# Kernel optimization log

Hardware: AMD Instinct MI355X
Metric: run time of the kernel (lower is better)

The kernel has to match this reference:

```python
import jax, jax.numpy as jnp
import numpy as np
from jax import lax

B, C, H, W = 4, 24, 128, 128
R = 7
NUM_CLASSES = 6
MAX_STEPS = 8


def _conv(x, w, b, pad):
    y = lax.conv_general_dilated(x, w, (1, 1), [(pad, pad), (pad, pad)],
                                 dimension_numbers=("NCHW", "OIHW", "NCHW"))
    return y + b[None, :, None, None]


def setup_inputs() -> dict:
    key = jax.random.key(0)
    ks = jax.random.split(key, 16)
    s = 0.05
    inp = {
        "depth_latent": jax.random.normal(ks[0], (B, C, H, W), jnp.float32),
        "texture_features": jax.random.normal(ks[1], (B, 3, H, W), jnp.float32),
        "class_labels": jax.random.randint(ks[2], (B,), 0, NUM_CLASSES),
        # texture_encoder
        "w_te1": jax.random.normal(ks[3], (64, 3, 3, 3), jnp.float32) * s,
        "b_te1": jnp.zeros((64,), jnp.float32),
        "w_te2": jax.random.normal(ks[4], (128, 64, 3, 3), jnp.float32) * s,
        "b_te2": jnp.zeros((128,), jnp.float32),
        # class embedding [num_classes, 128]
        "emb": jax.random.normal(ks[5], (NUM_CLASSES, 128), jnp.float32) * s,
        # fusion_layer: Conv2d(256,256,3) -> Conv2d(256, C*R*R, 1)
        "w_f1": jax.random.normal(ks[6], (256, 256, 3, 3), jnp.float32) * s,
        "b_f1": jnp.zeros((256,), jnp.float32),
        "w_f2": jax.random.normal(ks[7], (C * R * R, 256, 1, 1), jnp.float32) * s,
        "b_f2": jnp.zeros((C * R * R,), jnp.float32),
        # class_gate: Conv2d(128,64,3) -> Conv2d(64,num_classes,1)
        "w_g1": jax.random.normal(ks[8], (64, 128, 3, 3), jnp.float32) * s,
        "b_g1": jnp.zeros((64,), jnp.float32),
        "w_g2": jax.random.normal(ks[9], (NUM_CLASSES, 64, 1, 1), jnp.float32) * s,
        "b_g2": jnp.zeros((NUM_CLASSES,), jnp.float32),
        "class_intensity": jnp.ones((1, NUM_CLASSES, 1, 1), jnp.float32),
    }
    return inp


def _forward(depth_latent, texture_features, class_labels,
             w_te1, b_te1, w_te2, b_te2, emb,
             w_f1, b_f1, w_f2, b_f2,
             w_g1, b_g1, w_g2, b_g2, class_intensity):
    pad = R // 2
    # texture encoder
    tex = jax.nn.relu(_conv(texture_features, w_te1, b_te1, 1))
    tex = jax.nn.relu(_conv(tex, w_te2, b_te2, 1))  # [B,128,H,W]

    # 1-D integer class label path
    class_cond = jax.nn.one_hot(class_labels, NUM_CLASSES, dtype=jnp.float32)[:, :, None, None]  # [B,K,1,1]
    class_emb = emb[class_labels][:, :, None, None]  # [B,128,1,1]

    gate = jax.nn.sigmoid(_conv(jax.nn.relu(_conv(tex, w_g1, b_g1, 1)), w_g2, b_g2, 0))
    class_gate = gate * class_cond  # [B,K,H,W]

    fused = jnp.concatenate([tex, jnp.broadcast_to(class_emb, (tex.shape[0], 128, H, W))], axis=1)
    weights = _conv(jax.nn.relu(_conv(fused, w_f1, b_f1, 1)), w_f2, b_f2, 0)
    weights = weights.reshape(-1, C, R * R, H, W)

    intensity_map = (class_gate * class_intensity).sum(axis=1, keepdims=True)  # [B,1,H,W]
    weights = weights * intensity_map[:, :, None]  # [B,C,R*R,H,W]
    weights = jax.nn.softmax(weights, axis=2)

    def diffusion_step(lat):
        p = jnp.pad(lat, ((0, 0), (0, 0), (pad, pad), (pad, pad)), mode="edge")
        # unfold order: kernel row-major (i*R + j)
        windows = jnp.stack([p[:, :, i:i + H, j:j + W]
                             for i in range(R) for j in range(R)], axis=2)
        return (windows * weights).sum(axis=2)

    enhanced = lax.fori_loop(0, MAX_STEPS, lambda _, lat: diffusion_step(lat), depth_latent)

    condition_map = intensity_map * class_gate.sum(axis=1, keepdims=True)
    return enhanced, class_gate, condition_map


def reference(depth_latent, texture_features, class_labels,
              w_te1, b_te1, w_te2, b_te2, emb,
              w_f1, b_f1, w_f2, b_f2,
              w_g1, b_g1, w_g2, b_g2, class_intensity):
    return _forward(depth_latent, texture_features, class_labels,
                    w_te1, b_te1, w_te2, b_te2, emb,
                    w_f1, b_f1, w_f2, b_f2,
                    w_g1, b_g1, w_g2, b_g2, class_intensity)
```

## Files before the change

### kernel.cpp

```cpp
#include <hip/hip_runtime.h>
#include <hip/hip_bf16.h>
#include <stdint.h>

#define DINL __device__ __forceinline__

DINL float bf2f(__hip_bfloat16 v) { return __bfloat162float(v); }
DINL __hip_bfloat16 f2bf(float v) { return __float2bfloat16(v); }
DINL float bflo(unsigned int u) { return __uint_as_float(u << 16); }
DINL float bfhi(unsigned int u) { return __uint_as_float(u & 0xffff0000u); }

DINL float loadf(float v) { return v; }
DINL float loadf(__hip_bfloat16 v) { return __bfloat162float(v); }

typedef __attribute__((ext_vector_type(8))) short bf16x8;
typedef __attribute__((ext_vector_type(4))) float f32x4;

#define O_WTE1 0
#define O_WG2  1792
#define O_SS   2304
#define O_INT  11520
#define BO_W2B   308224u
#define BO_TE2B 1094656u
#define BO_WG1B 1242112u
#define BO_WF1B 1389568u
#define BO_TEX  4194304u
#define BO_F1   20971520u
#define BO_PING 54525952u
#define BO_PONG 60817408u
#define BO_W    67108864u
#define BO_T1   BO_W
#define BO_G1   (BO_W + 16777216u)

__global__ __launch_bounds__(256) void prep_kernel(
    const float* __restrict__ w_te1, const float* __restrict__ w_te2,
    const float* __restrict__ w_g1,  const float* __restrict__ w_f1,
    const float* __restrict__ w_f2,  const float* __restrict__ w_g2,
    const float* __restrict__ emb,   const int* __restrict__ labels,
    float* __restrict__ wsf)
{
  const int gid = blockIdx.x * 256 + threadIdx.x;
  const int stride = gridDim.x * 256;
  const int A0 = 1728, A1 = A0 + 393216, A2 = A1 + 73728, A3 = A2 + 73728,
            A4 = A3 + 294912, A5 = A4 + 384;
  __hip_bfloat16* w2b  = (__hip_bfloat16*)((char*)wsf + BO_W2B);
  __hip_bfloat16* te2b = (__hip_bfloat16*)((char*)wsf + BO_TE2B);
  __hip_bfloat16* g1b  = (__hip_bfloat16*)((char*)wsf + BO_WG1B);
  __hip_bfloat16* f1b  = (__hip_bfloat16*)((char*)wsf + BO_WF1B);
  for (int i = gid; i < A5; i += stride) {
    if (i < A0) {
      int s = i; int o = s / 27; int r = s - o * 27; int ic = r / 9; int t = r - ic * 9;
      wsf[O_WTE1 + (((o >> 5) * 3 + ic) * 9 + t) * 32 + (o & 31)] = w_te1[s];
    } else if (i < A1) {
      int s = i - A0;
      int j = s & 7; int lane = (s >> 3) & 63; int ks = (s >> 9) & 7;
      int mt = (s >> 12) & 3; int c = s >> 14;
      int tap = mt * 16 + (lane & 15);
      int k = ks * 32 + (lane >> 4) * 8 + j;
      float v = (tap < 49) ? w_f2[(c * 49 + tap) * 256 + k] : 0.f;
      w2b[s] = f2bf(v);
    } else if (i < A2) {
      int s = i - A1;
      int k = s & 31; int n = (s >> 5) & 63; int u = s >> 11;
      int t = u % 9; int v = u / 9; int kc = v & 1; int ocg = v >> 1;
      te2b[s] = f2bf(w_te2[((ocg * 64 + n) * 64 + kc * 32 + k) * 9 + t]);
    } else if (i < A3) {
      int s = i - A2;
      int k = s & 31; int n = (s >> 5) & 63; int u = s >> 11;
      int t = u % 9; int kc = u / 9;
      g1b[s] = f2bf(w_g1[(n * 128 + kc * 32 + k) * 9 + t]);
    } else if (i < A4) {
      int s = i - A3;
      int k = s & 31; int n = (s >> 5) & 63; int u = s >> 11;
      int t = u % 9; int v = u / 9; int kc = v & 3; int ocg = v >> 2;
      f1b[s] = f2bf(w_f1[((ocg * 64 + n) * 256 + kc * 32 + k) * 9 + t]);
    } else {
      int s = i - A4;
      wsf[O_WG2 + s] = w_g2[s];
    }
  }
  if (gid < 16384) {
    const int g = gid >> 4, slot = gid & 15;
    const int b = g >> 8, o = g & 255;
    const int lab = labels[b];
    float St[9];
#pragma unroll
    for (int t = 0; t < 9; ++t) St[t] = 0.f;
#pragma unroll 2
    for (int k = 0; k < 8; ++k) {
      const int i = slot * 8 + k;
      const float e = emb[lab * 128 + i];
      const float* wr = w_f1 + (size_t)(o * 256 + 128 + i) * 9;
#pragma unroll
      for (int t = 0; t < 9; ++t) St[t] += wr[t] * e;
    }
#pragma unroll
    for (int d = 1; d < 16; d <<= 1)
#pragma unroll
      for (int t = 0; t < 9; ++t) St[t] += __shfl_xor(St[t], d, 64);
    if (slot == 0) {
#pragma unroll
      for (int ch = 0; ch < 3; ++ch)
#pragma unroll
        for (int cw = 0; cw < 3; ++cw) {
          float sum = 0.f;
#pragma unroll
          for (int t = 0; t < 9; ++t) {
            int kh = t / 3, kw = t - kh * 3;
            bool ok = !(ch == 0 && kh == 0) && !(ch == 2 && kh == 2) &&
                      !(cw == 0 && kw == 0) && !(cw == 2 && kw == 2);
            if (ok) sum += St[t];
          }
          wsf[O_SS + g * 9 + ch * 3 + cw] = sum;
        }
    }
  }
}

template<typename TIn, int ICH, bool PIXMAJOR>
__global__ __launch_bounds__(256, 2) void conv3x3_kernel(
    const TIn* __restrict__ in, const float* __restrict__ wf,
    const float* __restrict__ bias,
    __hip_bfloat16* __restrict__ out, const int och_total)
{
  constexpr int CH = (ICH < 16) ? ICH : 16;
  constexpr int NCHUNK = ICH / CH;
  __shared__ TIn sIn[CH][18][20];
  const int tid = threadIdx.x;
  const int b = blockIdx.z;
  const int ob = blockIdx.y;
  const int och0 = ob * 32;
  const int tileY = blockIdx.x >> 3, tileX = blockIdx.x & 7;
  const int ty = tid >> 4, tx = tid & 15;
  const int h = tileY * 16 + ty, w = tileX * 16 + tx;
  const int h0 = tileY * 16 - 1, w0 = tileX * 16 - 1;

  float acc[32];
#pragma unroll
  for (int o = 0; o < 32; ++o) acc[o] = bias[och0 + o];

  for (int cc = 0; cc < NCHUNK; ++cc) {
    if (cc) __syncthreads();
    for (int e = tid; e < CH * 324; e += 256) {
      int ic = e / 324, r = e - ic * 324;
      int y = r / 18, x = r - y * 18;
      int gh = h0 + y, gw = w0 + x;
      TIn v = TIn(0.f);
      if ((unsigned)gh < 128u && (unsigned)gw < 128u)
        v = in[((b * ICH + cc * CH + ic) << 14) + (gh << 7) + gw];
      sIn[ic][y][x] = v;
    }
    __syncthreads();
#pragma unroll 1
    for (int ic = 0; ic < CH; ++ic) {
      const float* wrow = wf + (ob * ICH + cc * CH + ic) * 288;
#pragma unroll
      for (int t = 0; t < 9; ++t) {
        const int kh = t / 3, kw = t - kh * 3;
        const float v = loadf(sIn[ic][ty + kh][tx + kw]);
#pragma unroll
        for (int o = 0; o < 32; ++o)
          acc[o] = fmaf(wrow[t * 32 + o], v, acc[o]);
      }
    }
  }

  const int pix = (h << 7) + w;
  if constexpr (!PIXMAJOR) {
#pragma unroll
    for (int o = 0; o < 32; ++o)
      out[((b * och_total + och0 + o) << 14) + pix] = f2bf(fmaxf(acc[o], 0.f));
  } else {
    union { uint4 u4[4]; __hip_bfloat16 hh[32]; } pk;
#pragma unroll
    for (int o = 0; o < 32; ++o) pk.hh[o] = f2bf(fmaxf(acc[o], 0.f));
    uint4* dst = reinterpret_cast<uint4*>(out + ((size_t)(b << 14) + pix) * och_total + och0);
#pragma unroll
    for (int i = 0; i < 4; ++i) dst[i] = pk.u4[i];
  }
}

template<int ICH, bool ADD_SS>
__global__ __launch_bounds__(256, 2) void conv3x3_mfma_kernel(
    const __hip_bfloat16* __restrict__ in, const __hip_bfloat16* __restrict__ wb,
    const float* __restrict__ bias, const float* __restrict__ SS,
    __hip_bfloat16* __restrict__ out, const int och_total)
{
  constexpr int NKC = ICH / 32;
  __shared__ __hip_bfloat16 sH[324][40];
  __shared__ __hip_bfloat16 sW[9][64][40];
  const int tid = threadIdx.x, b = blockIdx.z, ocg = blockIdx.y;
  const int tileY = blockIdx.x >> 3, tileX = blockIdx.x & 7;
  const int h0 = tileY * 16 - 1, w0 = tileX * 16 - 1;
  const int wave = tid >> 6, lane = tid & 63, m16 = lane & 15, quad = lane >> 4;

  f32x4 acc[4][4];
#pragma unroll
  for (int i = 0; i < 4; ++i)
#pragma unroll
    for (int j = 0; j < 4; ++j) acc[i][j] = f32x4{0.f, 0.f, 0.f, 0.f};

  for (int kc = 0; kc < NKC; ++kc) {
    if (kc) __syncthreads();
    for (int e = tid; e < 1296; e += 256) {
      int pos = e >> 2, q = e & 3;
      int y = pos / 18, x = pos - y * 18;
      int gh = h0 + y, gw = w0 + x;
      uint4 v = uint4{0u, 0u, 0u, 0u};
      if ((unsigned)gh < 128u && (unsigned)gw < 128u)
        v = *(const uint4*)(in + ((size_t)((b << 14) + (gh << 7) + gw)) * ICH + kc * 32 + q * 8);
      *(uint4*)&sH[pos][q * 8] = v;
    }
    const uint4* wsrc = (const uint4*)(wb + ((size_t)(ocg * NKC + kc)) * 9 * 64 * 32);
    for (int e = tid; e < 2304; e += 256) {
      int q = e & 3, n = (e >> 2) & 63, t = e >> 8;
      *(uint4*)&sW[t][n][q * 8] = wsrc[e];
    }
    __syncthreads();
#pragma unroll
    for (int t = 0; t < 9; ++t) {
      const int dy = t / 3, dx = t - dy * 3;
      bf16x8 bfr[4];
#pragma unroll
      for (int nt = 0; nt < 4; ++nt)
        bfr[nt] = *(const bf16x8*)&sW[t][nt * 16 + m16][quad * 8];
#pragma unroll
      for (int mi = 0; mi < 4; ++mi) {
        const int py = wave * 4 + mi;
        const bf16x8 afr = *(const bf16x8*)&sH[(py + dy) * 18 + dx + m16][quad * 8];
#pragma unroll
        for (int nt = 0; nt < 4; ++nt)
          acc[mi][nt] = __builtin_amdgcn_mfma_f32_16x16x32_bf16(afr, bfr[nt], acc[mi][nt], 0, 0, 0);
      }
    }
  }

  float bv[4];
#pragma unroll
  for (int nt = 0; nt < 4; ++nt) bv[nt] = bias[ocg * 64 + nt * 16 + m16];
#pragma unroll
  for (int mi = 0; mi < 4; ++mi) {
    const int py = wave * 4 + mi;
    const int h = tileY * 16 + py;
    const int chc = (h == 0) ? 0 : ((h == 127) ? 2 : 1);
#pragma unroll
    for (int nt = 0; nt < 4; ++nt) {
      float sr0 = 0.f, sr1 = 0.f, sr2 = 0.f;
      if constexpr (ADD_SS) {
        const float* sp = SS + ((size_t)(b << 8) + (ocg * 64 + nt * 16 + m16)) * 9;
        sr0 = sp[chc * 3 + 0]; sr1 = sp[chc * 3 + 1]; sr2 = sp[chc * 3 + 2];
      }
      const int och = ocg * 64 + nt * 16 + m16;
#pragma unroll
      for (int r = 0; r < 4; ++r) {
        const int px = quad * 4 + r;
        const int w = tileX * 16 + px;
        float v = acc[mi][nt][r] + bv[nt];
        if constexpr (ADD_SS)
          v += (w == 0) ? sr0 : ((w == 127) ? sr2 : sr1);
        v = fmaxf(v, 0.f);
        out[((size_t)((b << 14) + (h << 7) + w)) * och_total + och] = f2bf(v);
      }
    }
  }
}

__global__ __launch_bounds__(256) void gate2_kernel(
    const __hip_bfloat16* __restrict__ g1, const float* __restrict__ wg2,
    const float* __restrict__ b_g2, const int* __restrict__ labels,
    const float* __restrict__ ci,
    float* __restrict__ out_cg, float* __restrict__ out_cond,
    float* __restrict__ inten)
{
  const int b = blockIdx.y;
  const int pix = blockIdx.x * 256 + threadIdx.x;
  float acc[6];
#pragma unroll
  for (int k = 0; k < 6; ++k) acc[k] = b_g2[k];
  const uint4* gp = (const uint4*)(g1 + ((size_t)((b << 14) + pix)) * 64);
#pragma unroll
  for (int i4 = 0; i4 < 8; ++i4) {
    const uint4 q = gp[i4];
    const float v0 = bflo(q.x), v1 = bfhi(q.x), v2 = bflo(q.y), v3 = bfhi(q.y);
    const float v4 = bflo(q.z), v5 = bfhi(q.z), v6 = bflo(q.w), v7 = bfhi(q.w);
#pragma unroll
    for (int k = 0; k < 6; ++k) {
      const float* wr = wg2 + k * 64 + i4 * 8;
      acc[k] = fmaf(wr[0], v0, acc[k]); acc[k] = fmaf(wr[1], v1, acc[k]);
      acc[k] = fmaf(wr[2], v2, acc[k]); acc[k] = fmaf(wr[3], v3, acc[k]);
      acc[k] = fmaf(wr[4], v4, acc[k]); acc[k] = fmaf(wr[5], v5, acc[k]);
      acc[k] = fmaf(wr[6], v6, acc[k]); acc[k] = fmaf(wr[7], v7, acc[k]);
    }
  }
  const int lab = labels[b];
  float gate[6], gl = 0.f;
#pragma unroll
  for (int k = 0; k < 6; ++k) {
    gate[k] = 1.f / (1.f + __expf(-acc[k]));
    gl = (k == lab) ? gate[k] : gl;
  }
  const float civ = ci[lab];
  const float it = gl * civ;
#pragma unroll
  for (int k = 0; k < 6; ++k)
    out_cg[((b * 6 + k) << 14) + pix] = (k == lab) ? gate[k] : 0.f;
  inten[(b << 14) + pix] = it;
  out_cond[(b << 14) + pix] = it * gl;
}

__global__ __launch_bounds__(256, 3) void gemm_softmax_kernel(
    const __hip_bfloat16* __restrict__ f1, const __hip_bfloat16* __restrict__ w2b,
    const float* __restrict__ b_f2, const float* __restrict__ inten,
    __hip_bfloat16* __restrict__ wout)
{
  __shared__ __hip_bfloat16 sW[2][8192];
  const int tid = threadIdx.x;
  const int pix0 = blockIdx.x * 128;
  const int c0 = blockIdx.y * 8;
  const int wave = tid >> 6, lane = tid & 63;
  const int n16 = lane & 15, quad = lane >> 4;
  const int p0 = pix0 + wave * 16 + n16;
  const int p1 = p0 + 64;

  bf16x8 bfr0[8], bfr1[8];
#pragma unroll
  for (int ks = 0; ks < 8; ++ks) {
    bfr0[ks] = *(const bf16x8*)(f1 + (size_t)p0 * 256 + ks * 32 + quad * 8);
    bfr1[ks] = *(const bf16x8*)(f1 + (size_t)p1 * 256 + ks * 32 + quad * 8);
  }

  const float s0v = inten[p0], s1v = inten[p1];
  const int ob0 = p0 >> 14, op0 = p0 & 16383;
  const int ob1 = p1 >> 14, op1 = p1 & 16383;

#define W2U(u) ((const uint4*)(w2b + ((((size_t)c0 + ((u) >> 1)) * 4 + (((u) & 1) << 1)) << 12)))

  {
    const uint4* s0 = W2U(0);
    uint4 t0[4];
#pragma unroll
    for (int j = 0; j < 4; ++j) t0[j] = s0[tid + j * 256];
    uint4* d0 = (uint4*)&sW[0][0];
#pragma unroll
    for (int j = 0; j < 4; ++j) d0[tid + j * 256] = t0[j];
  }
  __syncthreads();

#pragma unroll 1
  for (int cl = 0; cl < 8; ++cl) {
    const int c = c0 + cl;
    f32x4 ac0[4], ac1[4];
#pragma unroll
    for (int mt = 0; mt < 4; ++mt) { ac0[mt] = f32x4{0.f,0.f,0.f,0.f}; ac1[mt] = f32x4{0.f,0.f,0.f,0.f}; }

#pragma unroll
    for (int h = 0; h < 2; ++h) {
      const int u = cl * 2 + h;
      const uint4* sn = W2U(u < 15 ? u + 1 : 15);
      uint4 tn[4];
#pragma unroll
      for (int j = 0; j < 4; ++j) tn[j] = sn[tid + j * 256];

      const __hip_bfloat16* bufp = &sW[u & 1][0];
#pragma unroll
      for (int ks = 0; ks < 8; ++ks) {
        const bf16x8 a0 = *(const bf16x8*)(bufp + ((ks) * 64 + lane) * 8);
        const bf16x8 a1 = *(const bf16x8*)(bufp + ((8 + ks) * 64 + lane) * 8);
        ac0[h * 2 + 0] = __builtin_amdgcn_mfma_f32_16x16x32_bf16(a0, bfr0[ks], ac0[h * 2 + 0], 0, 0, 0);
        ac1[h * 2 + 0] = __builtin_amdgcn_mfma_f32_16x16x32_bf16(a0, bfr1[ks], ac1[h * 2 + 0], 0, 0, 0);
        ac0[h * 2 + 1] = __builtin_amdgcn_mfma_f32_16x16x32_bf16(a1, bfr0[ks], ac0[h * 2 + 1], 0, 0, 0);
        ac1[h * 2 + 1] = __builtin_amdgcn_mfma_f32_16x16x32_bf16(a1, bfr1[ks], ac1[h * 2 + 1], 0, 0, 0);
      }

      uint4* dn = (uint4*)&sW[(u + 1) & 1][0];
#pragma unroll
      for (int j = 0; j < 4; ++j) dn[tid + j * 256] = tn[j];
      __syncthreads();
    }

#pragma unroll
    for (int g = 0; g < 2; ++g) {
      f32x4* ac = g ? ac1 : ac0;
      const float s = g ? s1v : s0v;
      float mx = -3.4e38f;
#pragma unroll
      for (int mt = 0; mt < 4; ++mt)
#pragma unroll
        for (int r = 0; r < 4; ++r) {
          const int tap = mt * 16 + quad * 4 + r;
          const bool ok = tap < 49;
          const float lv = ok ? (ac[mt][r] + b_f2[c * 49 + (ok ? tap : 0)]) * s : -3.4e38f;
          ac[mt][r] = lv;
          mx = fmaxf(mx, lv);
        }
      mx = fmaxf(mx, __shfl_xor(mx, 16, 64));
      mx = fmaxf(mx, __shfl_xor(mx, 32, 64));
      float sum = 0.f;
#pragma unroll
      for (int mt = 0; mt < 4; ++mt)
#pragma unroll
        for (int r = 0; r < 4; ++r) {
          const float e = __expf(ac[mt][r] - mx);
          ac[mt][r] = e;
          sum += e;
        }
      sum += __shfl_xor(sum, 16, 64);
      sum += __shfl_xor(sum, 32, 64);
      const float rs = 1.f / sum;

      __hip_bfloat16* wo = wout + (((size_t)((g ? ob1 : ob0) * 24 + c) * 49) << 14) + (g ? op1 : op0);
#pragma unroll
      for (int mt = 0; mt < 4; ++mt)
#pragma unroll
        for (int r = 0; r < 4; ++r) {
          const int tap = mt * 16 + quad * 4 + r;
          if (tap < 49) wo[(size_t)tap << 14] = f2bf(ac[mt][r] * rs);
        }
    }
  }
#undef W2U
}

__global__ __launch_bounds__(256) void diff_kernel(
    const float* __restrict__ lin, const __hip_bfloat16* __restrict__ wts,
    float* __restrict__ lout)
{
  __shared__ float sT[14][136];
  const int bc = blockIdx.y;
  const int h0 = blockIdx.x * 8;
  const int tid = threadIdx.x;
  for (int e = tid; e < 14 * 134; e += 256) {
    int y = e / 134, x = e - y * 134;
    int gh = min(max(h0 - 3 + y, 0), 127), gw = min(max(x - 3, 0), 127);
    sT[y][x] = lin[(bc << 14) + (gh << 7) + gw];
  }
  __syncthreads();
  const int tw = (tid & 31) * 4;
  const int ty = tid >> 5;
  const int h = h0 + ty;
  const __hip_bfloat16* wp = wts + (((size_t)bc * 49) << 14) + (h << 7) + tw;
  float a0 = 0.f, a1 = 0.f, a2 = 0.f, a3 = 0.f;
#pragma unroll
  for (int kh = 0; kh < 7; ++kh) {
    const float* row = &sT[ty + kh][tw];
    float r[12];
    *(f32x4*)&r[0] = *(const f32x4*)(row);
    *(f32x4*)&r[4] = *(const f32x4*)(row + 4);
    *(f32x4*)&r[8] = *(const f32x4*)(row + 8);
#pragma unroll
    for (int kw = 0; kw < 7; ++kw) {
      const int t = kh * 7 + kw;
      const uint2 wq = *(const uint2*)(wp + ((size_t)t << 14));
      a0 = fmaf(bflo(wq.x), r[kw],     a0);
      a1 = fmaf(bfhi(wq.x), r[kw + 1], a1);
      a2 = fmaf(bflo(wq.y), r[kw + 2], a2);
      a3 = fmaf(bfhi(wq.y), r[kw + 3], a3);
    }
  }
  *(f32x4*)(lout + (bc << 14) + (h << 7) + tw) = f32x4{a0, a1, a2, a3};
}

extern "C" void kernel_launch(void* const* d_in, const int* in_sizes, int n_in,
                              void* d_out, int out_size, void* d_ws, size_t ws_size,
                              hipStream_t stream)
{
  const float* depth = (const float*)d_in[0];
  const float* texf  = (const float*)d_in[1];
  const int*   labels= (const int*)d_in[2];
  const float* w_te1 = (const float*)d_in[3];
  const float* b_te1 = (const float*)d_in[4];
  const float* w_te2 = (const float*)d_in[5];
  const float* b_te2 = (const float*)d_in[6];
  const float* emb   = (const float*)d_in[7];
  const float* w_f1  = (const float*)d_in[8];
  const float* b_f1  = (const float*)d_in[9];
  const float* w_f2  = (const float*)d_in[10];
  const float* b_f2  = (const float*)d_in[11];
  const float* w_g1  = (const float*)d_in[12];
  const float* b_g1  = (const float*)d_in[13];
  const float* w_g2  = (const float*)d_in[14];
  const float* b_g2  = (const float*)d_in[15];
  const float* ci    = (const float*)d_in[16];

  char*  ws  = (char*)d_ws;
  float* wsf = (float*)d_ws;
  __hip_bfloat16* w2bf  = (__hip_bfloat16*)(ws + BO_W2B);
  __hip_bfloat16* te2bf = (__hip_bfloat16*)(ws + BO_TE2B);
  __hip_bfloat16* g1bf  = (__hip_bfloat16*)(ws + BO_WG1B);
  __hip_bfloat16* f1bf  = (__hip_bfloat16*)(ws + BO_WF1B);
  __hip_bfloat16* tex   = (__hip_bfloat16*)(ws + BO_TEX);
  __hip_bfloat16* f1    = (__hip_bfloat16*)(ws + BO_F1);
  float* ping           = (float*)(ws + BO_PING);
  float* pong           = (float*)(ws + BO_PONG);
  __hip_bfloat16* wts   = (__hip_bfloat16*)(ws + BO_W);
  __hip_bfloat16* t1    = (__hip_bfloat16*)(ws + BO_T1);
  __hip_bfloat16* g1    = (__hip_bfloat16*)(ws + BO_G1);

  float* out      = (float*)d_out;
  float* out_enh  = out;
  float* out_cg   = out + 1572864;
  float* out_cond = out + 1966080;

  prep_kernel<<<512, 256, 0, stream>>>(w_te1, w_te2, w_g1, w_f1, w_f2, w_g2, emb, labels, wsf);
  conv3x3_kernel<float, 3, true><<<dim3(64, 2, 4), 256, 0, stream>>>(texf, wsf + O_WTE1, b_te1, t1, 64);
  conv3x3_mfma_kernel<64,  false><<<dim3(64, 2, 4), 256, 0, stream>>>(t1,  te2bf, b_te2, nullptr,      tex, 128);
  conv3x3_mfma_kernel<128, false><<<dim3(64, 1, 4), 256, 0, stream>>>(tex, g1bf,  b_g1,  nullptr,      g1,  64);
  gate2_kernel<<<dim3(64, 4), 256, 0, stream>>>(g1, wsf + O_WG2, b_g2, labels, ci, out_cg, out_cond, wsf + O_INT);
  conv3x3_mfma_kernel<128, true ><<<dim3(64, 4, 4), 256, 0, stream>>>(tex, f1bf,  b_f1,  wsf + O_SS,   f1,  256);
  gemm_softmax_kernel<<<dim3(512, 3), 256, 0, stream>>>(f1, w2bf, b_f2, wsf + O_INT, wts);

  dim3 dgrid(16, 96);
  diff_kernel<<<dgrid, 256, 0, stream>>>(depth, wts, ping);
  diff_kernel<<<dgrid, 256, 0, stream>>>(ping, wts, pong);
  diff_kernel<<<dgrid, 256, 0, stream>>>(pong, wts, ping);
  diff_kernel<<<dgrid, 256, 0, stream>>>(ping, wts, pong);
  diff_kernel<<<dgrid, 256, 0, stream>>>(pong, wts, ping);
  diff_kernel<<<dgrid, 256, 0, stream>>>(ping, wts, pong);
  diff_kernel<<<dgrid, 256, 0, stream>>>(pong, wts, ping);
  diff_kernel<<<dgrid, 256, 0, stream>>>(ping, wts, out_enh);
}
```

Measured before the change: 492.9 us.

## Fuse eight diffusion steps into one persistent kernel with whole-image LDS tile

Replaces eight separate diffusion launches with a single kernel where one 1024-thread block per (batch,channel) keeps the whole 128x128 latent in shared memory and iterates all steps, handling edge padding by clamping rows and replicating columns. This removes the intermediate global ping-pong traffic and the launch overhead between steps. The cost is that only 96 blocks run, leaving most compute units idle while the per-step weight stream is re-read from global memory.

Result: slower. 1.591 ms (+222.8%).

```diff
diff --git a/kernel.cpp b/kernel.cpp
--- a/kernel.cpp
+++ b/kernel.cpp
@@ -420,43 +420,76 @@
 #undef W2U
 }
 
-__global__ __launch_bounds__(256) void diff_kernel(
-    const float* __restrict__ lin, const __hip_bfloat16* __restrict__ wts,
-    float* __restrict__ lout)
-{
-  __shared__ float sT[14][136];
-  const int bc = blockIdx.y;
-  const int h0 = blockIdx.x * 8;
+__global__ __launch_bounds__(1024, 1) void diff_fused_kernel(
+    const float* __restrict__ depth, const __hip_bfloat16* __restrict__ wts,
+    float* __restrict__ out)
+{
+  __shared__ float sL[128][136];
+  const int bc = blockIdx.x;
   const int tid = threadIdx.x;
-  for (int e = tid; e < 14 * 134; e += 256) {
-    int y = e / 134, x = e - y * 134;
-    int gh = min(max(h0 - 3 + y, 0), 127), gw = min(max(x - 3, 0), 127);
-    sT[y][x] = lin[(bc << 14) + (gh << 7) + gw];
+  const float* din = depth + ((size_t)bc << 14);
+
+#pragma unroll
+  for (int i = 0; i < 16; ++i) {
+    const int e = tid + i * 1024;
+    const int r = e >> 7, c = e & 127;
+    const float v = din[e];
+    sL[r][c + 3] = v;
+    if (c == 0)   { sL[r][0] = v; sL[r][1] = v; sL[r][2] = v; }
+    if (c == 127) { sL[r][131] = v; sL[r][132] = v; sL[r][133] = v; }
   }
   __syncthreads();
-  const int tw = (tid & 31) * 4;
-  const int ty = tid >> 5;
-  const int h = h0 + ty;
-  const __hip_bfloat16* wp = wts + (((size_t)bc * 49) << 14) + (h << 7) + tw;
-  float a0 = 0.f, a1 = 0.f, a2 = 0.f, a3 = 0.f;
-#pragma unroll
-  for (int kh = 0; kh < 7; ++kh) {
-    const float* row = &sT[ty + kh][tw];
-    float r[12];
-    *(f32x4*)&r[0] = *(const f32x4*)(row);
-    *(f32x4*)&r[4] = *(const f32x4*)(row + 4);
-    *(f32x4*)&r[8] = *(const f32x4*)(row + 8);
-#pragma unroll
-    for (int kw = 0; kw < 7; ++kw) {
-      const int t = kh * 7 + kw;
-      const uint2 wq = *(const uint2*)(wp + ((size_t)t << 14));
-      a0 = fmaf(bflo(wq.x), r[kw],     a0);
-      a1 = fmaf(bfhi(wq.x), r[kw + 1], a1);
-      a2 = fmaf(bflo(wq.y), r[kw + 2], a2);
-      a3 = fmaf(bfhi(wq.y), r[kw + 3], a3);
-    }
-  }
-  *(f32x4*)(lout + (bc << 14) + (h << 7) + tw) = f32x4{a0, a1, a2, a3};
+
+  const __hip_bfloat16* wbase = wts + (((size_t)bc * 49) << 14);
+  float acc[4][4];
+
+#pragma unroll 1
+  for (int step = 0; step < 8; ++step) {
+#pragma unroll
+    for (int g = 0; g < 4; ++g) {
+      const int q = tid + g * 1024;
+      const int r = q >> 5, c0 = (q & 31) * 4;
+      float a0 = 0.f, a1 = 0.f, a2 = 0.f, a3 = 0.f;
+#pragma unroll
+      for (int kh = 0; kh < 7; ++kh) {
+        const int sr = min(max(r + kh - 3, 0), 127);
+        const float* row = &sL[sr][c0];
+        float rv[12];
+        *(f32x4*)&rv[0] = *(const f32x4*)(row);
+        *(f32x4*)&rv[4] = *(const f32x4*)(row + 4);
+        *(f32x4*)&rv[8] = *(const f32x4*)(row + 8);
+#pragma unroll
+        for (int kw = 0; kw < 7; ++kw) {
+          const int t = kh * 7 + kw;
+          const uint2 wq = *(const uint2*)(wbase + ((size_t)t << 14) + q * 4);
+          a0 = fmaf(bflo(wq.x), rv[kw],     a0);
+          a1 = fmaf(bfhi(wq.x), rv[kw + 1], a1);
+          a2 = fmaf(bflo(wq.y), rv[kw + 2], a2);
+          a3 = fmaf(bfhi(wq.y), rv[kw + 3], a3);
+        }
+      }
+      acc[g][0] = a0; acc[g][1] = a1; acc[g][2] = a2; acc[g][3] = a3;
+    }
+    if (step == 7) break;
+    __syncthreads();
+#pragma unroll
+    for (int g = 0; g < 4; ++g) {
+      const int q = tid + g * 1024;
+      const int r = q >> 5, c0 = (q & 31) * 4;
+      sL[r][c0 + 3] = acc[g][0]; sL[r][c0 + 4] = acc[g][1];
+      sL[r][c0 + 5] = acc[g][2]; sL[r][c0 + 6] = acc[g][3];
+      if ((q & 31) == 0)  { sL[r][0] = acc[g][0]; sL[r][1] = acc[g][0]; sL[r][2] = acc[g][0]; }
+      if ((q & 31) == 31) { sL[r][131] = acc[g][3]; sL[r][132] = acc[g][3]; sL[r][133] = acc[g][3]; }
+    }
+    __syncthreads();
+  }
+
+  float* dout = out + ((size_t)bc << 14);
+#pragma unroll
+  for (int g = 0; g < 4; ++g) {
+    const int q = tid + g * 1024;
+    *(f32x4*)(dout + q * 4) = *(f32x4*)&acc[g][0];
+  }
 }
 
 extern "C" void kernel_launch(void* const* d_in, const int* in_sizes, int n_in,
@@ -489,8 +522,6 @@
   __hip_bfloat16* f1bf  = (__hip_bfloat16*)(ws + BO_WF1B);
   __hip_bfloat16* tex   = (__hip_bfloat16*)(ws + BO_TEX);
   __hip_bfloat16* f1    = (__hip_bfloat16*)(ws + BO_F1);
-  float* ping           = (float*)(ws + BO_PING);
-  float* pong           = (float*)(ws + BO_PONG);
   __hip_bfloat16* wts   = (__hip_bfloat16*)(ws + BO_W);
   __hip_bfloat16* t1    = (__hip_bfloat16*)(ws + BO_T1);
   __hip_bfloat16* g1    = (__hip_bfloat16*)(ws + BO_G1);
@@ -508,13 +539,5 @@
   conv3x3_mfma_kernel<128, true ><<<dim3(64, 4, 4), 256, 0, stream>>>(tex, f1bf,  b_f1,  wsf + O_SS,   f1,  256);
   gemm_softmax_kernel<<<dim3(512, 3), 256, 0, stream>>>(f1, w2bf, b_f2, wsf + O_INT, wts);
 
-  dim3 dgrid(16, 96);
-  diff_kernel<<<dgrid, 256, 0, stream>>>(depth, wts, ping);
-  diff_kernel<<<dgrid, 256, 0, stream>>>(ping, wts, pong);
-  diff_kernel<<<dgrid, 256, 0, stream>>>(pong, wts, ping);
-  diff_kernel<<<dgrid, 256, 0, stream>>>(ping, wts, pong);
-  diff_kernel<<<dgrid, 256, 0, stream>>>(pong, wts, ping);
-  diff_kernel<<<dgrid, 256, 0, stream>>>(ping, wts, pong);
-  diff_kernel<<<dgrid, 256, 0, stream>>>(pong, wts, ping);
-  diff_kernel<<<dgrid, 256, 0, stream>>>(ping, wts, out_enh);
-}
+  diff_fused_kernel<<<96, 1024, 0, stream>>>(depth, wts, out_enh);
+}
```
